# Performance work log

Measured on AMD Instinct MI355X. Metric: run time of the kernel, lower is better.

## Reference

```python
import jax, jax.numpy as jnp
import numpy as np

K_MAX = 3
ITERS = 3
NEG_BIG = -1e9


def squash(x):
    # x: [..., O]
    sn = jnp.sum(jnp.square(x), axis=-1, keepdims=True)
    factor = sn / (1.0 + sn) / jnp.sqrt(sn + 1e-8)
    return factor * x


def setup_inputs() -> dict:
    key = jax.random.key(0)
    k1, k2, k3, k4 = jax.random.split(key, 4)
    N, L, D, O = 4096, 200, 64, 64
    behavior_embs = jax.random.normal(k1, (N, L, D), dtype=jnp.float32)
    W = jax.random.normal(k2, (D, O), dtype=jnp.float32)  # init_std=1.0
    routing_logits_init = jax.random.normal(k3, (N, K_MAX, L), dtype=jnp.float32)
    seq_len = jax.random.randint(k4, (N, 1), 0, L, dtype=jnp.int32)
    return {
        "behavior_embs": behavior_embs,
        "W": W,
        "routing_logits_init": routing_logits_init,
        "seq_len": seq_len,
    }


def reference(behavior_embs, W, routing_logits_init, seq_len):
    N, L, D = behavior_embs.shape
    # mask: [N, K_MAX, L] -- valid positions along L, tiled across capsules
    mask = jnp.arange(L)[None, None, :] < seq_len[:, None, :]  # [N,1,L]
    mask = jnp.broadcast_to(mask, (N, K_MAX, L))

    mappings = jnp.matmul(behavior_embs, W)          # [N, L, O]
    m_det = jax.lax.stop_gradient(mappings)         # routing uses detached mappings

    logits = routing_logits_init                     # [N, K_MAX, L]
    for _ in range(ITERS - 1):
        padded = jnp.where(mask, logits, NEG_BIG)
        # NOTE: softmax over the capsule dim (axis=1), as in the original
        weights = jax.nn.softmax(padded, axis=1)     # [N, K_MAX, L]
        candidates = jnp.matmul(weights, m_det)      # [N, K_MAX, O]
        interests = squash(candidates)
        logits = logits + jnp.einsum('nko,nlo->nkl', interests, m_det)

    padded = jnp.where(mask, logits, NEG_BIG)
    weights = jax.nn.softmax(padded, axis=1)
    candidates = jnp.matmul(weights, mappings)       # final iter uses non-detached
    interests = squash(candidates)                   # [N, K_MAX, O]
    return interests
```

## Files before the change

kernel.cpp:

```cpp
#include <hip/hip_runtime.h>
#include <math.h>

typedef _Float16 f16;
typedef _Float16 f16x8 __attribute__((ext_vector_type(8)));
typedef float f32x4 __attribute__((ext_vector_type(4)));

#define LSEQ 200
#define LT 13

__global__ __launch_bounds__(256, 5)
void capsule_kernel(const float* __restrict__ E,
                    const float* __restrict__ W,
                    const float* __restrict__ RL,
                    const int* __restrict__ SL,
                    float* __restrict__ out)
{
    __shared__ f16 m_sw[1792*8];
    __shared__ f16 w_c[3*224];
    __shared__ f16 i_c[3*80];
    __shared__ float cand[192];

    const int n = blockIdx.x;
    const int t = threadIdx.x;
    const int lane = t & 63;
    const int wv = t >> 6;
    const int q = lane >> 4;
    const int cc = lane & 15;
    const int cmin = cc < 3 ? cc : 2;

    const int o_own = wv*16 + cc;
    f16x8 wB[2];
    #pragma unroll
    for (int ks = 0; ks < 2; ks++) {
        f16x8 h;
        #pragma unroll
        for (int j = 0; j < 8; j++) h[j] = (f16)W[(ks*32 + q*8 + j)*64 + o_own];
        wB[ks] = h;
    }

    float lg[4][3];
    #pragma unroll
    for (int slot = 0; slot < 4; slot++) {
        int Tn = wv + slot*4;
        if (Tn < LT && lane < 16) {
            int l = Tn*16 + lane;
            if (l < LSEQ) {
                lg[slot][0] = RL[(size_t)n*600 + l];
                lg[slot][1] = RL[(size_t)n*600 + 200 + l];
                lg[slot][2] = RL[(size_t)n*600 + 400 + l];
            }
        }
    }
    const int s = SL[n];

    if (t < 9) {
        const f16x8 hz = {(f16)0.f,(f16)0.f,(f16)0.f,(f16)0.f,
                          (f16)0.f,(f16)0.f,(f16)0.f,(f16)0.f};
        int row = t / 3, off = 200 + (t % 3)*8;
        *(f16x8*)&w_c[row*224 + off] = hz;
    }

    const float* Eb = E + (size_t)n * (LSEQ*64);
    const float4 f4z = make_float4(0.f, 0.f, 0.f, 0.f);
    #pragma unroll
    for (int i = 0; i < 7; i++) {
        int g = t + i*256;
        int sb = g >> 6, c = g & 63;
        int Tl = sb >> 1, ks = sb & 1;
        int qq = c >> 4, m = c & 15;
        int l = Tl*16 + m;
        int kb = ks*32 + qq*8;
        float4 v0 = f4z, v1 = f4z;
        if (l < LSEQ) {
            v0 = *(const float4*)(Eb + l*64 + kb);
            v1 = *(const float4*)(Eb + l*64 + kb + 4);
        }
        f16x8 h = { (f16)v0.x,(f16)v0.y,(f16)v0.z,(f16)v0.w,
                    (f16)v1.x,(f16)v1.y,(f16)v1.z,(f16)v1.w };
        *(f16x8*)&m_sw[g*8] = h;
    }

    __syncthreads();

    f32x4 acc[LT];
    #pragma unroll
    for (int Tl = 0; Tl < LT; Tl++) {
        f32x4 c0 = {0.f, 0.f, 0.f, 0.f};
        #pragma unroll
        for (int ks = 0; ks < 2; ks++) {
            f16x8 a = *(f16x8*)&m_sw[((Tl*2 + ks)*64 + lane)*8];
            c0 = __builtin_amdgcn_mfma_f32_16x16x32_f16(a, wB[ks], c0, 0, 0, 0);
        }
        acc[Tl] = c0;
    }
    __syncthreads();

    const int kso = o_own >> 5, qo = (o_own & 31) >> 3, jo = o_own & 7;
    #pragma unroll
    for (int Tl = 0; Tl < LT; Tl++) {
        #pragma unroll
        for (int r = 0; r < 4; r++) {
            int lp = q*4 + r;
            m_sw[((Tl*2 + kso)*64 + qo*16 + lp)*8 + jo] = (f16)acc[Tl][r];
        }
    }
    #pragma unroll
    for (int slot = 0; slot < 4; slot++) {
        int Tn = wv + slot*4;
        if (Tn < LT && lane < 16) {
            int l = Tn*16 + lane;
            if (l < LSEQ) {
                float w0, w1, w2;
                if (l < s) {
                    float l0 = lg[slot][0], l1 = lg[slot][1], l2 = lg[slot][2];
                    float mx = fmaxf(fmaxf(l0, l1), l2);
                    float e0 = expf(l0 - mx), e1 = expf(l1 - mx), e2 = expf(l2 - mx);
                    float inv = 1.f / (e0 + e1 + e2);
                    w0 = e0*inv; w1 = e1*inv; w2 = e2*inv;
                } else {
                    w0 = w1 = w2 = (1.f/3.f);
                }
                w_c[l]       = (f16)w0;
                w_c[224 + l] = (f16)w1;
                w_c[448 + l] = (f16)w2;
            }
        }
    }
    __syncthreads();

    f16x8 mfrag[7];
    #pragma unroll
    for (int ks = 0; ks < 7; ks++) {
        f16x8 h;
        #pragma unroll
        for (int j = 0; j < 8; j++) {
            int l = ks*32 + q*8 + j;
            f16 v = (f16)0.f;
            if (l < 208) {
                int Tl = l >> 4, lp = l & 15;
                v = m_sw[((Tl*2 + kso)*64 + qo*16 + lp)*8 + jo];
            }
            h[j] = v;
        }
        mfrag[ks] = h;
    }

    for (int iter = 0; iter < 3; iter++) {
        f32x4 ca = {0.f, 0.f, 0.f, 0.f};
        #pragma unroll
        for (int ks = 0; ks < 7; ks++) {
            f16x8 b = *(f16x8*)&w_c[cmin*224 + ks*32 + q*8];
            ca = __builtin_amdgcn_mfma_f32_16x16x32_f16(mfrag[ks], b, ca, 0, 0, 0);
        }
        if (cc < 3) {
            #pragma unroll
            for (int r = 0; r < 4; r++) cand[cc*64 + wv*16 + q*4 + r] = ca[r];
        }
        __syncthreads();

        if (t < 192) {
            float x = cand[t];
            float sq = x*x;
            #pragma unroll
            for (int off = 32; off >= 1; off >>= 1) sq += __shfl_xor(sq, off, 64);
            float factor = sq / ((1.f + sq) * sqrtf(sq + 1e-8f));
            float y = factor * x;
            if (iter < 2) {
                i_c[(t >> 6)*80 + (t & 63)] = (f16)y;
            } else {
                out[(size_t)n*192 + t] = y;
            }
        }
        if (iter == 2) break;
        __syncthreads();

        f16x8 ia[2];
        ia[0] = *(f16x8*)&i_c[cmin*80 + q*8];
        ia[1] = *(f16x8*)&i_c[cmin*80 + 32 + q*8];
        #pragma unroll
        for (int slot = 0; slot < 4; slot++) {
            int Tn = wv + slot*4;
            if (Tn < LT) {
                f32x4 da = {0.f, 0.f, 0.f, 0.f};
                #pragma unroll
                for (int ko = 0; ko < 2; ko++) {
                    f16x8 b = *(f16x8*)&m_sw[((Tn*2 + ko)*64 + lane)*8];
                    da = __builtin_amdgcn_mfma_f32_16x16x32_f16(ia[ko], b, da, 0, 0, 0);
                }
                if (lane < 16) {
                    int l = Tn*16 + lane;
                    if (l < LSEQ) {
                        float w0, w1, w2;
                        if (l < s) {
                            float l0 = lg[slot][0] + da[0];
                            float l1 = lg[slot][1] + da[1];
                            float l2 = lg[slot][2] + da[2];
                            lg[slot][0] = l0; lg[slot][1] = l1; lg[slot][2] = l2;
                            float mx = fmaxf(fmaxf(l0, l1), l2);
                            float e0 = expf(l0 - mx), e1 = expf(l1 - mx), e2 = expf(l2 - mx);
                            float inv = 1.f / (e0 + e1 + e2);
                            w0 = e0*inv; w1 = e1*inv; w2 = e2*inv;
                        } else {
                            w0 = w1 = w2 = (1.f/3.f);
                        }
                        w_c[l]       = (f16)w0;
                        w_c[224 + l] = (f16)w1;
                        w_c[448 + l] = (f16)w2;
                    }
                }
            }
        }
        __syncthreads();
    }
}

extern "C" void kernel_launch(void* const* d_in, const int* in_sizes, int n_in,
                              void* d_out, int out_size, void* d_ws, size_t ws_size,
                              hipStream_t stream) {
    const float* E  = (const float*)d_in[0];
    const float* W  = (const float*)d_in[1];
    const float* RL = (const float*)d_in[2];
    const int*   SL = (const int*)d_in[3];
    float* o = (float*)d_out;
    const int N = in_sizes[3];
    capsule_kernel<<<dim3(N), dim3(256), 0, stream>>>(E, W, RL, SL, o);
}
```

Baseline: 302.8 us.

## Keep mappings in registers and reassociate agreement via W^T interests

Packs the MFMA accumulators of the mappings directly into register fragments with a permuted weight layout, which removes the shared-memory scatter of mappings and the gather back into fragments. The agreement step is reassociated as E·(W·interest): interests are first multiplied by a transposed W held in registers, then by the raw embeddings kept in shared memory. This saves LDS traffic and a barrier, but adds an extra small MFMA stage, another barrier, and a different rounding path through f16.

```diff
diff --git a/kernel.cpp b/kernel.cpp
--- a/kernel.cpp
+++ b/kernel.cpp
@@ -15,10 +15,11 @@
                     const int* __restrict__ SL,
                     float* __restrict__ out)
 {
-    __shared__ f16 m_sw[1792*8];
-    __shared__ f16 w_c[3*224];
-    __shared__ f16 i_c[3*80];
-    __shared__ float cand[192];
+    __shared__ __attribute__((aligned(16))) f16 e_sw[1792*8];
+    __shared__ __attribute__((aligned(16))) f16 w_p[3*224];
+    __shared__ __attribute__((aligned(16))) f16 i_c[3*80];
+    __shared__ __attribute__((aligned(16))) f16 iw_c[3*72];
+    __shared__ __attribute__((aligned(16))) float cand[192];
 
     const int n = blockIdx.x;
     const int t = threadIdx.x;
@@ -27,15 +28,20 @@
     const int q = lane >> 4;
     const int cc = lane & 15;
     const int cmin = cc < 3 ? cc : 2;
-
     const int o_own = wv*16 + cc;
-    f16x8 wB[2];
+
+    f16x8 wB[2], wT[2];
     #pragma unroll
     for (int ks = 0; ks < 2; ks++) {
         f16x8 h;
         #pragma unroll
         for (int j = 0; j < 8; j++) h[j] = (f16)W[(ks*32 + q*8 + j)*64 + o_own];
         wB[ks] = h;
+        const float4 a = *(const float4*)(W + o_own*64 + ks*32 + q*8);
+        const float4 b = *(const float4*)(W + o_own*64 + ks*32 + q*8 + 4);
+        f16x8 g = { (f16)a.x,(f16)a.y,(f16)a.z,(f16)a.w,
+                    (f16)b.x,(f16)b.y,(f16)b.z,(f16)b.w };
+        wT[ks] = g;
     }
 
     float lg[4][3];
@@ -53,11 +59,10 @@
     }
     const int s = SL[n];
 
-    if (t < 9) {
+    if (t < 12) {
         const f16x8 hz = {(f16)0.f,(f16)0.f,(f16)0.f,(f16)0.f,
                           (f16)0.f,(f16)0.f,(f16)0.f,(f16)0.f};
-        int row = t / 3, off = 200 + (t % 3)*8;
-        *(f16x8*)&w_c[row*224 + off] = hz;
+        *(f16x8*)&w_p[(t>>2)*224 + 192 + (t&3)*8] = hz;
     }
 
     const float* Eb = E + (size_t)n * (LSEQ*64);
@@ -77,7 +82,7 @@
         }
         f16x8 h = { (f16)v0.x,(f16)v0.y,(f16)v0.z,(f16)v0.w,
                     (f16)v1.x,(f16)v1.y,(f16)v1.z,(f16)v1.w };
-        *(f16x8*)&m_sw[g*8] = h;
+        *(f16x8*)&e_sw[g*8] = h;
     }
 
     __syncthreads();
@@ -88,22 +93,30 @@
         f32x4 c0 = {0.f, 0.f, 0.f, 0.f};
         #pragma unroll
         for (int ks = 0; ks < 2; ks++) {
-            f16x8 a = *(f16x8*)&m_sw[((Tl*2 + ks)*64 + lane)*8];
+            f16x8 a = *(f16x8*)&e_sw[((Tl*2 + ks)*64 + lane)*8];
             c0 = __builtin_amdgcn_mfma_f32_16x16x32_f16(a, wB[ks], c0, 0, 0, 0);
         }
         acc[Tl] = c0;
     }
-    __syncthreads();
-
-    const int kso = o_own >> 5, qo = (o_own & 31) >> 3, jo = o_own & 7;
-    #pragma unroll
-    for (int Tl = 0; Tl < LT; Tl++) {
+
+    f16x8 macc[7];
+    #pragma unroll
+    for (int p = 0; p < 6; p++) {
+        f16x8 h;
         #pragma unroll
         for (int r = 0; r < 4; r++) {
-            int lp = q*4 + r;
-            m_sw[((Tl*2 + kso)*64 + qo*16 + lp)*8 + jo] = (f16)acc[Tl][r];
-        }
-    }
+            h[r]     = (f16)acc[2*p][r];
+            h[4 + r] = (f16)acc[2*p + 1][r];
+        }
+        macc[p] = h;
+    }
+    {
+        f16x8 h;
+        #pragma unroll
+        for (int r = 0; r < 4; r++) { h[r] = (f16)acc[12][r]; h[4 + r] = (f16)0.f; }
+        macc[6] = h;
+    }
+
     #pragma unroll
     for (int slot = 0; slot < 4; slot++) {
         int Tn = wv + slot*4;
@@ -120,41 +133,25 @@
                 } else {
                     w0 = w1 = w2 = (1.f/3.f);
                 }
-                w_c[l]       = (f16)w0;
-                w_c[224 + l] = (f16)w1;
-                w_c[448 + l] = (f16)w2;
+                int wbase = (l>>5)*32 + (((l>>2)&3)<<3) + (((l>>4)&1)<<2) + (l&3);
+                w_p[wbase]       = (f16)w0;
+                w_p[224 + wbase] = (f16)w1;
+                w_p[448 + wbase] = (f16)w2;
             }
         }
     }
     __syncthreads();
-
-    f16x8 mfrag[7];
-    #pragma unroll
-    for (int ks = 0; ks < 7; ks++) {
-        f16x8 h;
-        #pragma unroll
-        for (int j = 0; j < 8; j++) {
-            int l = ks*32 + q*8 + j;
-            f16 v = (f16)0.f;
-            if (l < 208) {
-                int Tl = l >> 4, lp = l & 15;
-                v = m_sw[((Tl*2 + kso)*64 + qo*16 + lp)*8 + jo];
-            }
-            h[j] = v;
-        }
-        mfrag[ks] = h;
-    }
 
     for (int iter = 0; iter < 3; iter++) {
         f32x4 ca = {0.f, 0.f, 0.f, 0.f};
         #pragma unroll
-        for (int ks = 0; ks < 7; ks++) {
-            f16x8 b = *(f16x8*)&w_c[cmin*224 + ks*32 + q*8];
-            ca = __builtin_amdgcn_mfma_f32_16x16x32_f16(mfrag[ks], b, ca, 0, 0, 0);
-        }
-        if (cc < 3) {
+        for (int p = 0; p < 7; p++) {
+            f16x8 a = *(f16x8*)&w_p[cmin*224 + p*32 + q*8];
+            ca = __builtin_amdgcn_mfma_f32_16x16x32_f16(a, macc[p], ca, 0, 0, 0);
+        }
+        if (q == 0) {
             #pragma unroll
-            for (int r = 0; r < 4; r++) cand[cc*64 + wv*16 + q*4 + r] = ca[r];
+            for (int r = 0; r < 3; r++) cand[r*64 + o_own] = ca[r];
         }
         __syncthreads();
 
@@ -174,19 +171,30 @@
         if (iter == 2) break;
         __syncthreads();
 
-        f16x8 ia[2];
-        ia[0] = *(f16x8*)&i_c[cmin*80 + q*8];
-        ia[1] = *(f16x8*)&i_c[cmin*80 + 32 + q*8];
+        {
+            f16x8 ia0 = *(f16x8*)&i_c[cmin*80 + q*8];
+            f16x8 ia1 = *(f16x8*)&i_c[cmin*80 + 32 + q*8];
+            f32x4 dw = {0.f, 0.f, 0.f, 0.f};
+            dw = __builtin_amdgcn_mfma_f32_16x16x32_f16(ia0, wT[0], dw, 0, 0, 0);
+            dw = __builtin_amdgcn_mfma_f32_16x16x32_f16(ia1, wT[1], dw, 0, 0, 0);
+            if (q == 0) {
+                #pragma unroll
+                for (int r = 0; r < 3; r++) iw_c[r*72 + o_own] = (f16)dw[r];
+            }
+        }
+        __syncthreads();
+
+        f16x8 iwa0 = *(f16x8*)&iw_c[cmin*72 + q*8];
+        f16x8 iwa1 = *(f16x8*)&iw_c[cmin*72 + 32 + q*8];
         #pragma unroll
         for (int slot = 0; slot < 4; slot++) {
             int Tn = wv + slot*4;
             if (Tn < LT) {
                 f32x4 da = {0.f, 0.f, 0.f, 0.f};
-                #pragma unroll
-                for (int ko = 0; ko < 2; ko++) {
-                    f16x8 b = *(f16x8*)&m_sw[((Tn*2 + ko)*64 + lane)*8];
-                    da = __builtin_amdgcn_mfma_f32_16x16x32_f16(ia[ko], b, da, 0, 0, 0);
-                }
+                f16x8 b0 = *(f16x8*)&e_sw[((Tn*2 + 0)*64 + lane)*8];
+                da = __builtin_amdgcn_mfma_f32_16x16x32_f16(iwa0, b0, da, 0, 0, 0);
+                f16x8 b1 = *(f16x8*)&e_sw[((Tn*2 + 1)*64 + lane)*8];
+                da = __builtin_amdgcn_mfma_f32_16x16x32_f16(iwa1, b1, da, 0, 0, 0);
                 if (lane < 16) {
                     int l = Tn*16 + lane;
                     if (l < LSEQ) {
@@ -203,9 +211,10 @@
                         } else {
                             w0 = w1 = w2 = (1.f/3.f);
                         }
-                        w_c[l]       = (f16)w0;
-                        w_c[224 + l] = (f16)w1;
-                        w_c[448 + l] = (f16)w2;
+                        int wbase = (l>>5)*32 + (((l>>2)&3)<<3) + (((l>>4)&1)<<2) + (l&3);
+                        w_p[wbase]       = (f16)w0;
+                        w_p[224 + wbase] = (f16)w1;
+                        w_p[448 + wbase] = (f16)w2;
                     }
                 }
             }
```

New measurement: 442.9 us. 1.46x slower.
